# Optimization experiments

Hardware: AMD Instinct MI355X
Metric: run time of the kernel (lower is better)

Reference implementation:

```python
import math
import jax, jax.numpy as jnp
import numpy as np

C = 1.0          # Poincare ball curvature
NUM_HEADS = 8
EPS = 1e-15

def _beta(a, b):
    # Beta function via lgamma (python float constant)
    return math.exp(math.lgamma(a) + math.lgamma(b) - math.lgamma(a + b))

def h_linear(x, z, r, c=C):
    """HNN++ Poincare fully-connected layer (hypll HLinear).
    x: [..., in] points in the ball; z: [in, out] tangent weights; r: [out] bias."""
    sc = math.sqrt(c)
    x2 = jnp.sum(x * x, axis=-1, keepdims=True)
    lam = 2.0 / (1.0 - c * x2)                                # conformal factor
    zn = jnp.maximum(jnp.linalg.norm(z, axis=0), EPS)          # [out]
    inner = x @ z                                              # [..., out]
    two_scr = 2.0 * sc * r
    d = (2.0 * zn / sc) * jnp.arcsinh(
        (sc * inner * lam / zn) * jnp.cosh(two_scr) - (lam - 1.0) * jnp.sinh(two_scr)
    )
    w = jnp.sinh(sc * d) / sc
    return w / (1.0 + jnp.sqrt(1.0 + c * jnp.sum(w * w, axis=-1, keepdims=True)))

def pairwise_dist(q, k, c=C):
    """Poincare distance d(q,k) = arccosh(1 + 2c|q-k|^2 / ((1-c|q|^2)(1-c|k|^2))) / sqrt(c).
    q,k: [B,H,S,hd] -> [B,H,S,S]."""
    q2 = jnp.sum(q * q, axis=-1)
    k2 = jnp.sum(k * k, axis=-1)
    qk = jnp.einsum('bhqd,bhkd->bhqk', q, k)
    diff2 = jnp.maximum(q2[..., :, None] + k2[..., None, :] - 2.0 * qk, 0.0)
    denom = (1.0 - c * q2)[..., :, None] * (1.0 - c * k2)[..., None, :]
    arg = 1.0 + 2.0 * c * diff2 / denom
    return jnp.arccosh(jnp.maximum(arg, 1.0 + 1e-7)) / math.sqrt(c)

def midpoint(v, w, c=C):
    """Weighted Mobius gyromidpoint: m = 1/2 (x) (sum w*lam*x / sum w*(lam-1)).
    v: [B,H,Sk,hd], w: [B,H,Sq,Sk] -> [B,H,Sq,hd]."""
    v2 = jnp.sum(v * v, axis=-1)                      # [B,H,Sk]
    lam = 2.0 / (1.0 - c * v2)
    num = jnp.einsum('bhqk,bhkd->bhqd', w * lam[..., None, :], v)
    den = jnp.maximum(jnp.einsum('bhqk,bhk->bhq', w, lam - 1.0), EPS)[..., None]
    g = num / den                                     # gyromidpoint pre-scaling
    sc = math.sqrt(c)
    gn = jnp.maximum(jnp.linalg.norm(g, axis=-1, keepdims=True), EPS)
    t = jnp.tanh(0.5 * jnp.arctanh(jnp.clip(sc * gn, 0.0, 1.0 - 1e-7)))
    return (t / sc) * g / gn

def _forward(query, key, value, Wq, bq, Wk, bk, Wv, bv, scale_tau, scale_gamma):
    B, S, E = query.shape
    H = NUM_HEADS
    hd = E // H
    # hyperbolic q/k/v projections, then split into heads: [B,H,S,hd]
    q = h_linear(query, Wq, bq).reshape(B, S, H, hd).transpose(0, 2, 1, 3)
    k = h_linear(key, Wk, bk).reshape(B, S, H, hd).transpose(0, 2, 1, 3)
    v = h_linear(value, Wv, bv).reshape(B, S, H, hd).transpose(0, 2, 1, 3)
    # similarity = -dist/tau - gamma with tau = exp(-scale_tau)
    sim = -pairwise_dist(q, k) * jnp.exp(scale_tau[0]) - scale_gamma[0]
    causal = jnp.triu(jnp.ones((S, S), dtype=bool), k=1)
    sim = jnp.where(causal, -jnp.inf, sim)
    w = jnp.exp(sim)                                  # 'exp' attention activation
    agg = midpoint(v, w)                              # [B,H,S,hd]
    agg = agg.transpose(0, 2, 1, 3).reshape(B, S, E)
    # HNN++ beta-concatenation of the per-head ball points
    scale = _beta(E / 2.0, 0.5) / _beta(hd / 2.0, 0.5)
    return agg * scale

def setup_inputs() -> dict:
    root = jax.random.key(0)
    ks = jax.random.split(root, 8)
    B, S, E = 1, 2048, 512
    s = 0.02  # keep points well inside the unit ball
    return {
        'query': s * jax.random.normal(ks[0], (B, S, E), jnp.float32),
        'key':   s * jax.random.normal(ks[1], (B, S, E), jnp.float32),
        'value': s * jax.random.normal(ks[2], (B, S, E), jnp.float32),
        'Wq': s * jax.random.normal(ks[3], (E, E), jnp.float32),
        'Wk': s * jax.random.normal(ks[4], (E, E), jnp.float32),
        'Wv': s * jax.random.normal(ks[5], (E, E), jnp.float32),
        'bq': jnp.zeros((E,), jnp.float32),
        'bk': jnp.zeros((E,), jnp.float32),
        'bv': jnp.zeros((E,), jnp.float32),
        'scale_tau': jnp.zeros((1,), jnp.float32),
        'scale_gamma': jnp.zeros((1,), jnp.float32),
    }

def reference(query, key, value, Wq, Wk, Wv, bq, bk, bv, scale_tau, scale_gamma):
    return _forward(query, key, value, Wq, bq, Wk, bk, Wv, bv, scale_tau, scale_gamma)
```

## Files before the change

### kernel.cpp

```cpp
#include <hip/hip_runtime.h>
#include <cmath>

#define H 8
#define SEQ 2048
#define EDIM 512
#define HD 64
#define EPSF 1e-15f

typedef short bf16x8 __attribute__((ext_vector_type(8)));
typedef float f32x4 __attribute__((ext_vector_type(4)));

#define ZN_OFF    16
#define ACC_OFF   (ZN_OFF + 3 * EDIM)
#define STATS_OFF (ACC_OFF + H * SEQ * 80)
#define CQ_OFF    (STATS_OFF + 3 * H * SEQ)
#define IK_OFF    (CQ_OFF + H * SEQ)
#define U16_OFF   (IK_OFF + H * SEQ + 16)
#define WT_U16    0
#define QKVB_U16  (WT_U16 + 3 * EDIM * EDIM)
#define VT_U16    (QKVB_U16 + 3 * SEQ * EDIM)

__device__ __forceinline__ float bf2f(unsigned short u){
  union { unsigned int i; float f; } v; v.i = ((unsigned int)u) << 16; return v.f;
}
__device__ __forceinline__ unsigned short f2bf(float f){
  union { float f; unsigned int i; } v; v.f = f;
  unsigned int x = v.i;
  unsigned int r = (x + 0x7fffu + ((x >> 16) & 1u)) >> 16;
  return (unsigned short)r;
}

__device__ __forceinline__ int detect_f32(const unsigned short* __restrict__ q){
  const int l = threadIdx.x & 63;
  float mx = 0.f;
  #pragma unroll
  for (int j = 0; j < 4; ++j) mx = fmaxf(mx, fabsf(bf2f(q[l * 4 + j])));
  #pragma unroll
  for (int m = 32; m >= 1; m >>= 1) mx = fmaxf(mx, __shfl_xor(mx, m, 64));
  return mx > 1000.f;
}

__global__ __launch_bounds__(256) void wcvt_kernel(
    const void* __restrict__ Wq, const void* __restrict__ Wk, const void* __restrict__ Wv,
    const unsigned short* __restrict__ qprobe,
    unsigned short* __restrict__ WT, float* __restrict__ zn)
{
  const int p = blockIdx.y;
  const int bi = blockIdx.x >> 3, bo = blockIdx.x & 7;
  const void* W = (p == 0) ? Wq : ((p == 1) ? Wk : Wv);
  const int t = threadIdx.x;
  const int isf32 = detect_f32(qprobe);
  __shared__ float tile[64][65];

  #pragma unroll
  for (int j = 0; j < 16; ++j){
    int idx = t + 256 * j;
    int il = idx >> 6, ol = idx & 63;
    float val;
    if (isf32) val = ((const float*)W)[(size_t)(bi * 64 + il) * EDIM + bo * 64 + ol];
    else       val = bf2f(((const unsigned short*)W)[(size_t)(bi * 64 + il) * EDIM + bo * 64 + ol]);
    tile[il][ol] = val;
  }
  __syncthreads();
  if (t < 64){
    float s = 0.f;
    #pragma unroll 8
    for (int i = 0; i < 64; ++i){ float v = tile[i][t]; s += v * v; }
    atomicAdd(&zn[p * EDIM + bo * 64 + t], s);
  }
  #pragma unroll
  for (int j = 0; j < 16; ++j){
    int idx = t + 256 * j;
    int ol = idx >> 6, il = idx & 63;
    WT[((size_t)p * EDIM + bo * 64 + ol) * EDIM + bi * 64 + il] = f2bf(tile[il][ol]);
  }
}

__global__ __launch_bounds__(256) void hlinear_kernel(
    const void* __restrict__ Xq, const void* __restrict__ Xk, const void* __restrict__ Xv,
    const unsigned short* __restrict__ WT,
    const void* __restrict__ Bq, const void* __restrict__ Bk, const void* __restrict__ Bv,
    const float* __restrict__ znacc,
    unsigned short* __restrict__ qkvb, float* __restrict__ stats,
    float* __restrict__ cqs, float* __restrict__ iks,
    unsigned short* __restrict__ VT)
{
  const int p = blockIdx.y;
  const void* X  = (p == 0) ? Xq : ((p == 1) ? Xk : Xv);
  const void* Bb = (p == 0) ? Bq : ((p == 1) ? Bk : Bv);
  const int r0 = blockIdx.x * 16;
  const int t  = threadIdx.x;
  const int w = t >> 6, lane = t & 63;
  const int col = lane & 15, quad = lane >> 4;
  const int isf32 = detect_f32((const unsigned short*)Xq);

  __shared__ float smem[16 * EDIM];
  __shared__ float sw2[16];

  const unsigned short* WTb = WT + ((size_t)p * EDIM + w * 128 + col) * EDIM;
  const float* Xf = (const float*)X + (size_t)(r0 + col) * EDIM;
  const unsigned short* Xh = (const unsigned short*)X + (size_t)(r0 + col) * EDIM;

  f32x4 acc[8];
  #pragma unroll
  for (int nt = 0; nt < 8; ++nt) acc[nt] = (f32x4){0.f, 0.f, 0.f, 0.f};
  float x2part = 0.f;

  for (int ks = 0; ks < 16; ++ks){
    bf16x8 af;
    if (isf32){
      float4 xa = *(const float4*)&Xf[ks * 32 + quad * 8];
      float4 xb = *(const float4*)&Xf[ks * 32 + quad * 8 + 4];
      float xv[8] = {xa.x, xa.y, xa.z, xa.w, xb.x, xb.y, xb.z, xb.w};
      #pragma unroll
      for (int j = 0; j < 8; ++j){ af[j] = (short)f2bf(xv[j]); x2part += xv[j] * xv[j]; }
    } else {
      af = *(const bf16x8*)&Xh[ks * 32 + quad * 8];
      #pragma unroll
      for (int j = 0; j < 8; ++j){ float xv = bf2f((unsigned short)af[j]); x2part += xv * xv; }
    }
    #pragma unroll
    for (int nt = 0; nt < 8; ++nt){
      bf16x8 bf = *(const bf16x8*)&WTb[(size_t)nt * 16 * EDIM + ks * 32 + quad * 8];
      acc[nt] = __builtin_amdgcn_mfma_f32_16x16x32_bf16(af, bf, acc[nt], 0, 0, 0);
    }
  }
  x2part += __shfl_xor(x2part, 16, 64);
  x2part += __shfl_xor(x2part, 32, 64);
  float lamr[4], lm1[4];
  #pragma unroll
  for (int r = 0; r < 4; ++r){
    float x2r = __shfl(x2part, quad * 4 + r, 64);
    lamr[r] = 2.f / (1.f - x2r);
    lm1[r] = lamr[r] - 1.f;
  }
  #pragma unroll
  for (int nt = 0; nt < 8; ++nt){
    const int n = w * 128 + nt * 16 + col;
    float znv = fmaxf(sqrtf(znacc[p * EDIM + n]), EPSF);
    float rb;
    if (isf32) rb = ((const float*)Bb)[n];
    else       rb = bf2f(((const unsigned short*)Bb)[n]);
    float e2r = __expf(2.f * rb);
    float ie2r = 1.f / e2r;
    float ch = 0.5f * (e2r + ie2r), sh = 0.5f * (e2r - ie2r);
    float izn = 1.f / znv;
    float tz = 2.f * znv;
    #pragma unroll
    for (int r = 0; r < 4; ++r){
      float a = (acc[nt][r] * lamr[r] * izn) * ch - lm1[r] * sh;
      float b = a + sqrtf(a * a + 1.f);
      float tt = __expf(tz * __logf(b));
      smem[(quad * 4 + r) * EDIM + n] = 0.5f * (tt - 1.f / tt);
    }
  }
  __syncthreads();

  {
    int row = t >> 4, l = t & 15;
    float s = 0.f;
    for (int o = l; o < EDIM; o += 16){ float wv = smem[row * EDIM + o]; s += wv * wv; }
    #pragma unroll
    for (int m = 8; m >= 1; m >>= 1) s += __shfl_xor(s, m, 16);
    if (l == 0) sw2[row] = s;
  }
  __syncthreads();

  const int o0 = 2 * t;
  const int h0 = t >> 5;
  const int d0 = o0 & 63;
  const int l5 = t & 31;
  #pragma unroll
  for (int rr = 0; rr < 16; ++rr){
    float inv = 1.f / (1.f + sqrtf(1.f + sw2[rr]));
    unsigned short b0 = f2bf(smem[rr * EDIM + o0] * inv);
    unsigned short b1 = f2bf(smem[rr * EDIM + o0 + 1] * inv);
    float r0v = bf2f(b0), r1v = bf2f(b1);
    int s = r0 + rr;
    unsigned int* dst = (unsigned int*)&qkvb[(((size_t)p * H + h0) * SEQ + s) * HD + d0];
    *dst = (unsigned int)b0 | ((unsigned int)b1 << 16);
    float ss = r0v * r0v + r1v * r1v;
    #pragma unroll
    for (int m = 16; m >= 1; m >>= 1) ss += __shfl_xor(ss, m, 64);
    if (p == 2){
      float lam = 2.f / (1.f - ss);
      VT[((size_t)h0 * 80 + d0) * SEQ + s]     = f2bf(r0v * lam);
      VT[((size_t)h0 * 80 + d0 + 1) * SEQ + s] = f2bf(r1v * lam);
      if (l5 < 16)
        VT[((size_t)h0 * 80 + 64 + l5) * SEQ + s] = (l5 == 0) ? f2bf(lam - 1.f) : 0;
    }
    if (l5 == 0){
      stats[((size_t)p * H + h0) * SEQ + s] = ss;
      if (p == 0) cqs[(size_t)h0 * SEQ + s] = 2.f / (1.f - ss);
      if (p == 1) iks[(size_t)h0 * SEQ + s] = 1.f / (1.f - ss);
    }
  }
}

__global__ __launch_bounds__(256) void attn_kernel(
    const unsigned short* __restrict__ Qb, const unsigned short* __restrict__ Kb,
    const unsigned short* __restrict__ VT,
    const float* __restrict__ q2s_all, const float* __restrict__ k2s_all,
    const float* __restrict__ cqs_all, const float* __restrict__ iks_all,
    const void* __restrict__ tau, const void* __restrict__ gam,
    const unsigned short* __restrict__ qprobe,
    float* __restrict__ ACC)
{
  const int h  = blockIdx.y;
  const int tile = blockIdx.x >> 3;
  const int sl = blockIdx.x & 7;
  if (sl > tile) return;
  const int t = threadIdx.x;
  const int w = t >> 6, lane = t & 63;
  const int col = lane & 15, quad = lane >> 4;
  const int q0 = tile * 64 + w * 16;

  const unsigned short* Qh  = Qb + (size_t)h * SEQ * HD;
  const unsigned short* Kh  = Kb + (size_t)h * SEQ * HD;
  const unsigned short* VTh = VT + (size_t)h * 80 * SEQ;
  const float* q2s = q2s_all + (size_t)h * SEQ;
  const float* k2s = k2s_all + (size_t)h * SEQ;
  const float* cqs = cqs_all + (size_t)h * SEQ;
  const float* iks = iks_all + (size_t)h * SEQ;

  const int isf32 = detect_f32(qprobe);
  float tauv, gamv;
  if (isf32){ tauv = ((const float*)tau)[0]; gamv = ((const float*)gam)[0]; }
  else      { tauv = bf2f(((const unsigned short*)tau)[0]);
              gamv = bf2f(((const unsigned short*)gam)[0]); }
  const float e_tau = __expf(tauv);

  const int srcA = ((quad & 1) * 2) * 16 + col;
  const int srcB = srcA + 16;
  const int tsel = quad >> 1;

  bf16x8 qf0 = *(const bf16x8*)&Qh[(size_t)(q0 + col) * HD + quad * 8];
  bf16x8 qf1 = *(const bf16x8*)&Qh[(size_t)(q0 + col) * HD + 32 + quad * 8];
  const float q2 = q2s[q0 + col];
  const float cq = cqs[q0 + col];
  const int qmax = q0 + col;

  f32x4 pv[5];
  #pragma unroll
  for (int nt = 0; nt < 5; ++nt) pv[nt] = (f32x4){0.f, 0.f, 0.f, 0.f};

  const int nch = ((tile - sl) >> 3) + 1;
  const int nhalf = nch * 2;
  int kb32 = sl * 64;

  bf16x8 ckf0[2], ckf1[2], nkf0[2], nkf1[2];
  float4 ck2[2], cik[2], nk2[2], nik[2];
  #pragma unroll
  for (int tt = 0; tt < 2; ++tt){
    const int kbase = kb32 + 16 * tt;
    ckf0[tt] = *(const bf16x8*)&Kh[(size_t)(kbase + col) * HD + quad * 8];
    ckf1[tt] = *(const bf16x8*)&Kh[(size_t)(kbase + col) * HD + 32 + quad * 8];
    ck2[tt]  = *(const float4*)&k2s[kbase + quad * 4];
    cik[tt]  = *(const float4*)&iks[kbase + quad * 4];
  }

  for (int i = 0; i < nhalf; ++i){
    const int nkb32 = (i & 1) ? (kb32 + 512 - 32) : (kb32 + 32);
    const bool have_next = (i + 1 < nhalf);
    if (have_next){
      #pragma unroll
      for (int tt = 0; tt < 2; ++tt){
        const int kbase = nkb32 + 16 * tt;
        nkf0[tt] = *(const bf16x8*)&Kh[(size_t)(kbase + col) * HD + quad * 8];
        nkf1[tt] = *(const bf16x8*)&Kh[(size_t)(kbase + col) * HD + 32 + quad * 8];
        nk2[tt]  = *(const float4*)&k2s[kbase + quad * 4];
        nik[tt]  = *(const float4*)&iks[kbase + quad * 4];
      }
    }

    unsigned int tlo[2], thi[2];
    #pragma unroll
    for (int tt = 0; tt < 2; ++tt){
      const int kbase = kb32 + 16 * tt;
      f32x4 s = (f32x4){0.f, 0.f, 0.f, 0.f};
      s = __builtin_amdgcn_mfma_f32_16x16x32_bf16(ckf0[tt], qf0, s, 0, 0, 0);
      s = __builtin_amdgcn_mfma_f32_16x16x32_bf16(ckf1[tt], qf1, s, 0, 0, 0);
      unsigned short pb[4];
      #pragma unroll
      for (int r = 0; r < 4; ++r){
        float k2 = (r == 0) ? ck2[tt].x : (r == 1) ? ck2[tt].y : (r == 2) ? ck2[tt].z : ck2[tt].w;
        float ik = (r == 0) ? cik[tt].x : (r == 1) ? cik[tt].y : (r == 2) ? cik[tt].z : cik[tt].w;
        float diff2 = fmaxf(q2 + k2 - 2.f * s[r], 0.f);
        float u = fmaxf(diff2 * cq * ik, 1e-7f);
        float z = 1.f + u + sqrtf(u * (u + 2.f));
        float dist = __logf(z);
        float wv = __expf(-e_tau * dist - gamv);
        int key = kbase + quad * 4 + r;
        if (key > qmax) wv = 0.f;
        pb[r] = f2bf(wv);
      }
      tlo[tt] = (unsigned int)pb[0] | ((unsigned int)pb[1] << 16);
      thi[tt] = (unsigned int)pb[2] | ((unsigned int)pb[3] << 16);
    }
    unsigned int a0 = (unsigned int)__shfl((int)tlo[0], srcA, 64);
    unsigned int a1 = (unsigned int)__shfl((int)tlo[1], srcA, 64);
    unsigned int b0 = (unsigned int)__shfl((int)thi[0], srcA, 64);
    unsigned int b1 = (unsigned int)__shfl((int)thi[1], srcA, 64);
    unsigned int c0 = (unsigned int)__shfl((int)tlo[0], srcB, 64);
    unsigned int c1 = (unsigned int)__shfl((int)tlo[1], srcB, 64);
    unsigned int d0 = (unsigned int)__shfl((int)thi[0], srcB, 64);
    unsigned int d1 = (unsigned int)__shfl((int)thi[1], srcB, 64);
    union { uint4 u; bf16x8 v; } pw;
    pw.u.x = tsel ? a1 : a0;
    pw.u.y = tsel ? b1 : b0;
    pw.u.z = tsel ? c1 : c0;
    pw.u.w = tsel ? d1 : d0;
    #pragma unroll
    for (int nt = 0; nt < 5; ++nt){
      bf16x8 vf = *(const bf16x8*)&VTh[(size_t)(16 * nt + col) * SEQ + kb32 + quad * 8];
      pv[nt] = __builtin_amdgcn_mfma_f32_16x16x32_bf16(pw.v, vf, pv[nt], 0, 0, 0);
    }

    if (have_next){
      #pragma unroll
      for (int tt = 0; tt < 2; ++tt){
        ckf0[tt] = nkf0[tt]; ckf1[tt] = nkf1[tt];
        ck2[tt] = nk2[tt];   cik[tt] = nik[tt];
      }
    }
    kb32 = nkb32;
  }

  #pragma unroll
  for (int r = 0; r < 4; ++r){
    float* row = ACC + ((size_t)h * SEQ + q0 + quad * 4 + r) * 80;
    #pragma unroll
    for (int nt = 0; nt < 5; ++nt)
      atomicAdd(&row[16 * nt + col], pv[nt][r]);
  }
}

__global__ __launch_bounds__(64) void attn_fin_kernel(
    const float* __restrict__ ACC, float* __restrict__ out, float beta_scale)
{
  const int h = blockIdx.y, tile = blockIdx.x;
  const int t = threadIdx.x;
  const int col = t & 15, quad = t >> 4;
  const int q0 = tile * 16;

  f32x4 pv[5];
  #pragma unroll
  for (int nt = 0; nt < 5; ++nt)
    #pragma unroll
    for (int r = 0; r < 4; ++r)
      pv[nt][r] = ACC[((size_t)h * SEQ + q0 + quad * 4 + r) * 80 + 16 * nt + col];

  #pragma unroll
  for (int r = 0; r < 4; ++r){
    float den = __shfl(pv[4][r], quad * 16, 64);
    den = fmaxf(den, EPSF);
    float inv_den = 1.f / den;
    float g[4];
    float gsq = 0.f;
    #pragma unroll
    for (int nt = 0; nt < 4; ++nt){ g[nt] = pv[nt][r] * inv_den; gsq += g[nt] * g[nt]; }
    #pragma unroll
    for (int m = 8; m >= 1; m >>= 1) gsq += __shfl_xor(gsq, m, 64);
    float gn = fmaxf(sqrtf(gsq), EPSF);
    float x = fminf(gn, 1.f - 1e-7f);
    float tt2 = x / (1.f + sqrtf(1.f - x * x));
    float scl = (tt2 / gn) * beta_scale;
    const int q = q0 + quad * 4 + r;
    #pragma unroll
    for (int nt = 0; nt < 4; ++nt)
      out[(size_t)q * EDIM + h * HD + 16 * nt + col] = g[nt] * scl;
  }
}

extern "C" void kernel_launch(void* const* d_in, const int* in_sizes, int n_in,
                              void* d_out, int out_size, void* d_ws, size_t ws_size,
                              hipStream_t stream){
  const void* Xq  = d_in[0];
  const void* Xk  = d_in[1];
  const void* Xv  = d_in[2];
  const void* Wq  = d_in[3];
  const void* Wk  = d_in[4];
  const void* Wv  = d_in[5];
  const void* Bq  = d_in[6];
  const void* Bk  = d_in[7];
  const void* Bv  = d_in[8];
  const void* tau = d_in[9];
  const void* gam = d_in[10];

  float* wsf   = (float*)d_ws;
  float* zn    = wsf + ZN_OFF;
  float* ACC   = wsf + ACC_OFF;
  float* stats = wsf + STATS_OFF;
  float* cqs   = wsf + CQ_OFF;
  float* iks   = wsf + IK_OFF;
  unsigned short* u16b = (unsigned short*)(wsf + U16_OFF);
  unsigned short* WT   = u16b + WT_U16;
  unsigned short* qkvb = u16b + QKVB_U16;
  unsigned short* VT   = u16b + VT_U16;

  unsigned short* Qb = qkvb;
  unsigned short* Kb = qkvb + (size_t)H * SEQ * HD;
  float* q2s = stats;
  float* k2s = stats + (size_t)H * SEQ;
  const unsigned short* qprobe = (const unsigned short*)Xq;

  double lb1 = lgamma(EDIM / 2.0) + lgamma(0.5) - lgamma(EDIM / 2.0 + 0.5);
  double lb2 = lgamma(HD / 2.0)   + lgamma(0.5) - lgamma(HD / 2.0 + 0.5);
  float beta_scale = (float)exp(lb1 - lb2);

  hipMemsetAsync(zn, 0, (size_t)(3 * EDIM + H * SEQ * 80) * sizeof(float), stream);
  wcvt_kernel<<<dim3(64, 3), dim3(256), 0, stream>>>(Wq, Wk, Wv, qprobe, WT, zn);
  hlinear_kernel<<<dim3(SEQ / 16, 3), dim3(256), 0, stream>>>(
      Xq, Xk, Xv, WT, Bq, Bk, Bv, zn, qkvb, stats, cqs, iks, VT);
  attn_kernel<<<dim3(32 * 8, H), dim3(256), 0, stream>>>(
      Qb, Kb, VT, q2s, k2s, cqs, iks, tau, gam, qprobe, ACC);
  attn_fin_kernel<<<dim3(128, H), dim3(64), 0, stream>>>(
      ACC, (float*)d_out, beta_scale);
}
```

Measured before the change: 213.3 us.

## Replace atomic split-K accumulation with per-slice partial buffers reduced in finalizer

Each attention split-K slice now writes its partial MFMA accumulators as coalesced float4 stores into a dedicated slot, and the finalize kernel sums the valid slices itself. This removes float atomics on the shared accumulator and the large memset that zeroed it. In exchange it needs a much larger workspace and makes the finalizer read up to eight partials per tile. The old atomic path is kept as a fallback when the workspace is too small.

Result: no change. 215.3 us (+0.9%).

```diff
diff --git a/kernel.cpp b/kernel.cpp
--- a/kernel.cpp
+++ b/kernel.cpp
@@ -11,14 +11,17 @@
 typedef float f32x4 __attribute__((ext_vector_type(4)));
 
 #define ZN_OFF    16
-#define ACC_OFF   (ZN_OFF + 3 * EDIM)
-#define STATS_OFF (ACC_OFF + H * SEQ * 80)
+#define STATS_OFF (ZN_OFF + 3 * EDIM)
 #define CQ_OFF    (STATS_OFF + 3 * H * SEQ)
 #define IK_OFF    (CQ_OFF + H * SEQ)
 #define U16_OFF   (IK_OFF + H * SEQ + 16)
 #define WT_U16    0
 #define QKVB_U16  (WT_U16 + 3 * EDIM * EDIM)
 #define VT_U16    (QKVB_U16 + 3 * SEQ * EDIM)
+#define U16_TOTAL (VT_U16 + H * 80 * SEQ)
+#define BIG_OFF   (U16_OFF + U16_TOTAL / 2 + 16)
+#define PART_FLOATS (8 * 32 * 8 * 4 * 320 * 4)
+#define ACC_FLOATS  (H * SEQ * 80)
 
 __device__ __forceinline__ float bf2f(unsigned short u){
   union { unsigned int i; float f; } v; v.i = ((unsigned int)u) << 16; return v.f;
@@ -204,7 +207,7 @@
     const float* __restrict__ cqs_all, const float* __restrict__ iks_all,
     const void* __restrict__ tau, const void* __restrict__ gam,
     const unsigned short* __restrict__ qprobe,
-    float* __restrict__ ACC)
+    float* __restrict__ big, int use_part)
 {
   const int h  = blockIdx.y;
   const int tile = blockIdx.x >> 3;
@@ -326,29 +329,55 @@
     kb32 = nkb32;
   }
 
-  #pragma unroll
-  for (int r = 0; r < 4; ++r){
-    float* row = ACC + ((size_t)h * SEQ + q0 + quad * 4 + r) * 80;
+  if (use_part){
+    float4* slot = (float4*)big +
+        (size_t)(((((h * 32 + tile) * 8) + sl) * 4 + w)) * 320;
     #pragma unroll
     for (int nt = 0; nt < 5; ++nt)
-      atomicAdd(&row[16 * nt + col], pv[nt][r]);
+      slot[nt * 64 + lane] = (float4){pv[nt][0], pv[nt][1], pv[nt][2], pv[nt][3]};
+  } else {
+    #pragma unroll
+    for (int r = 0; r < 4; ++r){
+      float* row = big + ((size_t)h * SEQ + q0 + quad * 4 + r) * 80;
+      #pragma unroll
+      for (int nt = 0; nt < 5; ++nt)
+        atomicAdd(&row[16 * nt + col], pv[nt][r]);
+    }
   }
 }
 
 __global__ __launch_bounds__(64) void attn_fin_kernel(
-    const float* __restrict__ ACC, float* __restrict__ out, float beta_scale)
+    const float* __restrict__ big, int use_part,
+    float* __restrict__ out, float beta_scale)
 {
-  const int h = blockIdx.y, tile = blockIdx.x;
+  const int h = blockIdx.y, tile16 = blockIdx.x;
   const int t = threadIdx.x;
   const int col = t & 15, quad = t >> 4;
-  const int q0 = tile * 16;
+  const int q0 = tile16 * 16;
 
   f32x4 pv[5];
   #pragma unroll
-  for (int nt = 0; nt < 5; ++nt)
-    #pragma unroll
-    for (int r = 0; r < 4; ++r)
-      pv[nt][r] = ACC[((size_t)h * SEQ + q0 + quad * 4 + r) * 80 + 16 * nt + col];
+  for (int nt = 0; nt < 5; ++nt) pv[nt] = (f32x4){0.f, 0.f, 0.f, 0.f};
+
+  if (use_part){
+    const int st = tile16 >> 2, w = tile16 & 3;
+    const int nv = (st + 1 < 8) ? st + 1 : 8;
+    for (int sl = 0; sl < nv; ++sl){
+      const float4* slot = (const float4*)big +
+          (size_t)(((((h * 32 + st) * 8) + sl) * 4 + w)) * 320;
+      #pragma unroll
+      for (int nt = 0; nt < 5; ++nt){
+        float4 v = slot[nt * 64 + t];
+        pv[nt][0] += v.x; pv[nt][1] += v.y; pv[nt][2] += v.z; pv[nt][3] += v.w;
+      }
+    }
+  } else {
+    #pragma unroll
+    for (int nt = 0; nt < 5; ++nt)
+      #pragma unroll
+      for (int r = 0; r < 4; ++r)
+        pv[nt][r] = big[((size_t)h * SEQ + q0 + quad * 4 + r) * 80 + 16 * nt + col];
+  }
 
   #pragma unroll
   for (int r = 0; r < 4; ++r){
@@ -389,7 +418,6 @@
 
   float* wsf   = (float*)d_ws;
   float* zn    = wsf + ZN_OFF;
-  float* ACC   = wsf + ACC_OFF;
   float* stats = wsf + STATS_OFF;
   float* cqs   = wsf + CQ_OFF;
   float* iks   = wsf + IK_OFF;
@@ -397,6 +425,9 @@
   unsigned short* WT   = u16b + WT_U16;
   unsigned short* qkvb = u16b + QKVB_U16;
   unsigned short* VT   = u16b + VT_U16;
+  float* big   = wsf + BIG_OFF;
+
+  const int use_part = (ws_size >= (size_t)(BIG_OFF + PART_FLOATS) * sizeof(float)) ? 1 : 0;
 
   unsigned short* Qb = qkvb;
   unsigned short* Kb = qkvb + (size_t)H * SEQ * HD;
@@ -408,12 +439,14 @@
   double lb2 = lgamma(HD / 2.0)   + lgamma(0.5) - lgamma(HD / 2.0 + 0.5);
   float beta_scale = (float)exp(lb1 - lb2);
 
-  hipMemsetAsync(zn, 0, (size_t)(3 * EDIM + H * SEQ * 80) * sizeof(float), stream);
+  hipMemsetAsync(zn, 0, (size_t)(3 * EDIM) * sizeof(float), stream);
+  if (!use_part)
+    hipMemsetAsync(big, 0, (size_t)ACC_FLOATS * sizeof(float), stream);
   wcvt_kernel<<<dim3(64, 3), dim3(256), 0, stream>>>(Wq, Wk, Wv, qprobe, WT, zn);
   hlinear_kernel<<<dim3(SEQ / 16, 3), dim3(256), 0, stream>>>(
       Xq, Xk, Xv, WT, Bq, Bk, Bv, zn, qkvb, stats, cqs, iks, VT);
   attn_kernel<<<dim3(32 * 8, H), dim3(256), 0, stream>>>(
-      Qb, Kb, VT, q2s, k2s, cqs, iks, tau, gam, qprobe, ACC);
+      Qb, Kb, VT, q2s, k2s, cqs, iks, tau, gam, qprobe, big, use_part);
   attn_fin_kernel<<<dim3(128, H), dim3(64), 0, stream>>>(
-      ACC, (float*)d_out, beta_scale);
-}
+      big, use_part, (float*)d_out, beta_scale);
+}
```
